# Optimization experiments

Measured on AMD Instinct MI355X. Metric: run time of the kernel, lower is better.

Reference implementation:

```python
import jax, jax.numpy as jnp
import numpy as np

IOU_THR = 0.5
SCORE_THR = 0.5
MAX_DET = 100
B, N, C = 16, 25200, 80


def setup_inputs() -> dict:
    key = jax.random.key(0)
    k1, k2, k3 = jax.random.split(key, 3)
    return {
        "boxes_xywh": jax.random.uniform(k1, (B, N, 4), dtype=jnp.float32),
        "objectness": jax.random.uniform(k2, (B, N, 1), dtype=jnp.float32),
        "class_prob": jax.random.uniform(k3, (B, N, C), dtype=jnp.float32),
    }


def _xywh_to_corners(b):
    x, y, w, h = jnp.split(b, 4, axis=-1)
    return jnp.concatenate([x - w / 2, y - h / 2, x + w / 2, y + h / 2], axis=-1)


def _broadcast_iou(box, boxes):
    # box [4], boxes [N,4] in x1,y1,x2,y2
    lt = jnp.maximum(box[:2], boxes[:, :2])
    rb = jnp.minimum(box[2:], boxes[:, 2:])
    wh = jnp.clip(rb - lt, 0.0)
    inter = wh[:, 0] * wh[:, 1]
    a1 = (box[2] - box[0]) * (box[3] - box[1])
    a2 = (boxes[:, 2] - boxes[:, 0]) * (boxes[:, 3] - boxes[:, 1])
    return inter / (a1 + a2 - inter + 1e-9)


def _nms_single(cand):
    # cand: [N, 4+1+C] rows = (x1,y1,x2,y2, score, class_probs...)
    n, d = cand.shape
    scores = cand[:, 4]
    active0 = scores >= SCORE_THR

    def body(i, state):
        active, out, count = state
        masked = jnp.where(active, scores, -jnp.inf)
        best = jnp.argmax(masked)
        valid = jnp.any(active)
        best_box = cand[best]
        out = out.at[i].set(jnp.where(valid, best_box, out[i]))
        count = count + valid.astype(jnp.int32)
        iou = _broadcast_iou(best_box[:4], cand[:, :4])
        keep = active & (iou <= IOU_THR)
        keep = keep.at[best].set(False)
        active = jnp.where(valid, keep, active)
        return active, out, count

    out0 = jnp.zeros((MAX_DET, d), cand.dtype)
    _, out, count = jax.lax.fori_loop(0, MAX_DET, body, (active0, out0, jnp.int32(0)))
    return out, count


def reference(boxes_xywh, objectness, class_prob):
    corners = _xywh_to_corners(boxes_xywh)  # [B,N,4]
    combined = jnp.concatenate([corners, objectness, class_prob], axis=-1)  # [B,N,5+C]
    final_result, count = jax.vmap(_nms_single)(combined)  # [B,MAX_DET,5+C], [B]
    nms_boxes = final_result[..., 0:4]
    nms_scores = final_result[..., 4:5]
    nms_classes = final_result[..., 5:]
    valid_count = count.astype(jnp.int32)[:, None]  # [B,1]
    return nms_boxes, nms_scores, nms_classes, valid_count
```

## Files before the change

kernel.cpp:

```cpp
#include <hip/hip_runtime.h>

#define NBOX    25200
#define NQ4     6300
#define NBATCH  16
#define NCLS    80
#define MAXDET  100
#define NBUCKET 1024
#define CAP     13824
#define SCORE_THR 0.5f
#define IOU_THR   0.5f
#define NGROUP  16
#define LAZY_BKT 896

__device__ __forceinline__ void mk_corners(float x, float y, float w, float h,
                                           float& x1, float& y1, float& x2, float& y2) {
#pragma clang fp contract(off)
    float hw = w * 0.5f;
    float hh = h * 0.5f;
    x1 = x - hw; y1 = y - hh; x2 = x + hw; y2 = y + hh;
}

__device__ __forceinline__ float areaf(float x1, float y1, float x2, float y2) {
#pragma clang fp contract(off)
    return (x2 - x1) * (y2 - y1);
}

__device__ __forceinline__ bool iou_gt(float kx1, float ky1, float kx2, float ky2, float ka,
                                       float cx1, float cy1, float cx2, float cy2, float ca) {
#pragma clang fp contract(off)
    float lx = fmaxf(kx1, cx1);
    float ly = fmaxf(ky1, cy1);
    float rx = fminf(kx2, cx2);
    float ry = fminf(ky2, cy2);
    float w  = fmaxf(rx - lx, 0.0f);
    float h  = fmaxf(ry - ly, 0.0f);
    float inter = w * h;
    float denom = ka + ca - inter + 1e-9f;
    return (inter / denom) > IOU_THR;
}

__device__ __forceinline__ float readlane_f(float v, int j) {
    return __uint_as_float((unsigned)__builtin_amdgcn_readlane((int)__float_as_uint(v), j));
}

__device__ __forceinline__ unsigned score_key(float s) {
    return __float_as_uint(s) - 0x3F000000u;
}

__global__ __launch_bounds__(1024)
void nms_kernel(const float* __restrict__ boxes_xywh,
                const float* __restrict__ objectness,
                const float* __restrict__ class_prob,
                float* __restrict__ out) {
    __shared__ unsigned s_hist[NBUCKET];
    __shared__ unsigned s_start[NBUCKET];
    __shared__ unsigned s_a[CAP];
    __shared__ unsigned s_b[CAP];
    __shared__ float4   s_kbox[MAXDET];
    __shared__ unsigned s_kept_idx[MAXDET];
    __shared__ unsigned s_wsum[16];
    __shared__ unsigned s_woff[16];
    __shared__ int      s_count;

    const int b = blockIdx.x;
    const int t = threadIdx.x;
    const int w = t >> 6;
    const int l = t & 63;
    const float* obj = objectness + (size_t)b * NBOX;
    const float* bx  = boxes_xywh + (size_t)b * NBOX * 4;

    float4 r[7];
#pragma unroll
    for (int i = 0; i < 7; ++i) {
        int n4 = t + (i << 10);
        if (n4 < NQ4) r[i] = *(const float4*)(obj + n4 * 4);
    }

    s_hist[t] = 0u;
    __syncthreads();
#pragma unroll
    for (int i = 0; i < 7; ++i) {
        int n4 = t + (i << 10);
        if (n4 < NQ4) {
            float sv[4] = {r[i].x, r[i].y, r[i].z, r[i].w};
#pragma unroll
            for (int u = 0; u < 4; ++u) {
                if (sv[u] >= SCORE_THR) {
                    unsigned bkt = score_key(sv[u]) >> 13;
                    if (bkt > 1023u) bkt = 1023u;
                    atomicAdd(&s_hist[bkt], 1u);
                }
            }
        }
    }
    __syncthreads();

    {
        unsigned f = s_hist[1023 - t];
        unsigned v = f;
#pragma unroll
        for (int off = 1; off < 64; off <<= 1) {
            unsigned u = (unsigned)__shfl_up((int)v, off);
            if (l >= off) v += u;
        }
        if (l == 63) s_wsum[w] = v;
        __syncthreads();
        if (t < 64) {
            unsigned x = (t < 16) ? s_wsum[t] : 0u;
            unsigned y = x;
#pragma unroll
            for (int off = 1; off < 16; off <<= 1) {
                unsigned u = (unsigned)__shfl_up((int)y, off);
                if (t >= off) y += u;
            }
            if (t < 16) s_woff[t] = y - x;
        }
        __syncthreads();
        s_start[1023 - t] = v - f + s_woff[w];
    }
    if (t == 0) s_count = 0;
    __syncthreads();

#pragma unroll
    for (int i = 0; i < 7; ++i) {
        int n4 = t + (i << 10);
        if (n4 < NQ4) {
            float sv[4] = {r[i].x, r[i].y, r[i].z, r[i].w};
#pragma unroll
            for (int u = 0; u < 4; ++u) {
                if (sv[u] >= SCORE_THR) {
                    unsigned ekey = score_key(sv[u]);
                    unsigned bkt  = ekey >> 13;
                    if (bkt > 1023u) bkt = 1023u;
                    if (bkt >= LAZY_BKT) {
                        int n = n4 * 4 + u;
                        unsigned el = ekey & 0x1FFFu;
                        unsigned pos = atomicAdd(&s_start[bkt], 1u);
                        if (pos < CAP)
                            s_a[pos] = (el << 18) | (0x3FFFFu - (unsigned)n);
                    }
                }
            }
        }
    }
    __syncthreads();

    auto sort_bucket = [&](int bkt) {
        unsigned h = s_hist[bkt];
        if (h == 0u) return;
        unsigned end = s_start[bkt];
        unsigned hi  = (end > CAP) ? CAP : end;
        unsigned lo  = (end >= h) ? end - h : 0u;
        if (lo > hi) lo = hi;
        unsigned sz = hi - lo;
        if (sz == 0u) return;
        if (sz <= 64u) {
            unsigned v = (l < (int)sz) ? s_a[lo + (unsigned)l] : 0u;
            int rank = 0;
            for (unsigned j = 0; j < sz; ++j)
                rank += ((unsigned)__shfl((int)v, (int)j) > v) ? 1 : 0;
            if (l < (int)sz) s_b[lo + (unsigned)rank] = v;
        } else {
            for (unsigned bb = 0; bb < sz; bb += 64u) {
                bool valid = bb + (unsigned)l < sz;
                unsigned v = valid ? s_a[lo + bb + (unsigned)l] : 0u;
                int rank = 0;
                for (unsigned j = 0; j < sz; ++j)
                    rank += (s_a[lo + j] > v) ? 1 : 0;
                if (valid) s_b[lo + (unsigned)rank] = v;
            }
        }
    };

    for (int bkt = (1023 - 63) + w; bkt <= 1023; bkt += 16) sort_bucket(bkt);
    __syncthreads();

    int count = 0;
    int nscat = 2;
    for (int g = 0; g < NGROUP; ++g) {
        const int BH = 1023 - (g << 6);
        const int BL = BH - 63;

        if (g >= nscat) {
            for (int n4 = t; n4 < NQ4; n4 += 1024) {
                float4 s4 = *(const float4*)(obj + n4 * 4);
                float sv[4] = {s4.x, s4.y, s4.z, s4.w};
#pragma unroll
                for (int u = 0; u < 4; ++u) {
                    if (sv[u] >= SCORE_THR) {
                        unsigned ekey = score_key(sv[u]);
                        unsigned bkt  = ekey >> 13;
                        if (bkt > 1023u) bkt = 1023u;
                        if (bkt < LAZY_BKT) {
                            int n = n4 * 4 + u;
                            unsigned el = ekey & 0x1FFFu;
                            unsigned pos = atomicAdd(&s_start[bkt], 1u);
                            if (pos < CAP)
                                s_a[pos] = (el << 18) | (0x3FFFFu - (unsigned)n);
                        }
                    }
                }
            }
            __syncthreads();
            nscat = NGROUP;
            for (int bkt = BL + w; bkt <= BH; bkt += 16) sort_bucket(bkt);
            __syncthreads();
        }

        if (w == 0) {
            unsigned glo = (g == 0) ? 0u : s_start[BH + 1];
            unsigned ghi = s_start[BL];
            if (glo > CAP) glo = CAP;
            if (ghi > CAP) ghi = CAP;

            if (glo < ghi && count < MAXDET) {
                unsigned aidx, bidx; float4 aq, bq; float asc, bsc;
                auto loadc = [&](unsigned cb, unsigned& ix, float4& q, float& sc) {
                    ix = 0u; q = make_float4(0.f, 0.f, 0.f, 0.f); sc = 0.f;
                    unsigned p0 = cb + (unsigned)l;
                    if (p0 < ghi) {
                        unsigned p = s_b[p0];
                        ix = 0x3FFFFu - (p & 0x3FFFFu);
                        q = *(const float4*)(bx + (size_t)ix * 4);
                        sc = obj[ix];
                    }
                };
                loadc(glo, aidx, aq, asc);
                loadc(glo + 64u, bidx, bq, bsc);

                for (unsigned base = glo; base < ghi && count < MAXDET; base += 64u) {
                    unsigned cidx = aidx; float4 cq = aq; float csc = asc;
                    aidx = bidx; aq = bq; asc = bsc;
                    loadc(base + 128u, bidx, bq, bsc);

                    int m = (int)(ghi - base); if (m > 64) m = 64;
                    float cx1, cy1, cx2, cy2;
                    mk_corners(cq.x, cq.y, cq.z, cq.w, cx1, cy1, cx2, cy2);
                    float ca = areaf(cx1, cy1, cx2, cy2);

                    bool sup = (l >= m);
                    int k = 0;
                    for (; k + 4 <= count; k += 4) {
                        float4 kb0 = s_kbox[k],     kb1 = s_kbox[k + 1];
                        float4 kb2 = s_kbox[k + 2], kb3 = s_kbox[k + 3];
                        sup = sup | iou_gt(kb0.x, kb0.y, kb0.z, kb0.w,
                                           areaf(kb0.x, kb0.y, kb0.z, kb0.w), cx1, cy1, cx2, cy2, ca);
                        sup = sup | iou_gt(kb1.x, kb1.y, kb1.z, kb1.w,
                                           areaf(kb1.x, kb1.y, kb1.z, kb1.w), cx1, cy1, cx2, cy2, ca);
                        sup = sup | iou_gt(kb2.x, kb2.y, kb2.z, kb2.w,
                                           areaf(kb2.x, kb2.y, kb2.z, kb2.w), cx1, cy1, cx2, cy2, ca);
                        sup = sup | iou_gt(kb3.x, kb3.y, kb3.z, kb3.w,
                                           areaf(kb3.x, kb3.y, kb3.z, kb3.w), cx1, cy1, cx2, cy2, ca);
                    }
                    for (; k < count; ++k) {
                        float4 kb = s_kbox[k];
                        sup = sup | iou_gt(kb.x, kb.y, kb.z, kb.w,
                                           areaf(kb.x, kb.y, kb.z, kb.w), cx1, cy1, cx2, cy2, ca);
                    }
                    unsigned long long act = __ballot(!sup);

                    unsigned long long accmask = 0ull;
                    const int cbase = count;
                    while (act != 0ull && count < MAXDET) {
                        int j = (int)__builtin_ctzll(act);
                        accmask |= 1ull << j;
                        float bx1 = readlane_f(cx1, j), by1 = readlane_f(cy1, j);
                        float bx2 = readlane_f(cx2, j), by2 = readlane_f(cy2, j);
                        float bar = readlane_f(ca, j);
                        bool su = iou_gt(bx1, by1, bx2, by2, bar, cx1, cy1, cx2, cy2, ca);
                        ++count;
                        act &= ~(1ull << j);
                        act &= ~__ballot(su);
                    }

                    if (accmask & (1ull << l)) {
                        int slot = cbase + (int)__popcll(accmask & ((1ull << l) - 1ull));
                        s_kbox[slot] = make_float4(cx1, cy1, cx2, cy2);
                        s_kept_idx[slot] = cidx;
                        float* ob = out + ((size_t)b * MAXDET + slot) * 4;
                        ob[0] = cx1; ob[1] = cy1; ob[2] = cx2; ob[3] = cy2;
                        out[NBATCH * MAXDET * 4 + b * MAXDET + slot] = csc;
                    }
                    __asm__ volatile("s_waitcnt lgkmcnt(0)" ::: "memory");
                }
            }
            if (l == 0) s_count = count;
        } else if (g + 1 < NGROUP && g + 1 < nscat) {
            const int BH2 = BH - 64, BL2 = BH2 - 63;
            for (int bkt = BL2 + (w - 1); bkt <= BH2; bkt += 15) sort_bucket(bkt);
        }
        __syncthreads();
        if (s_count >= MAXDET) break;
    }

    const int cf = s_count;
    for (int e = t; e < MAXDET * 4; e += 1024) {
        if ((e >> 2) >= cf) out[(size_t)b * MAXDET * 4 + e] = 0.0f;
    }
    for (int i = t; i < MAXDET; i += 1024) {
        if (i >= cf) out[NBATCH * MAXDET * 4 + b * MAXDET + i] = 0.0f;
    }
    const float* cp = class_prob + (size_t)b * NBOX * NCLS;
    float* oc = out + NBATCH * MAXDET * 5 + (size_t)b * MAXDET * NCLS;
    for (int e = t; e < cf * NCLS; e += 1024) {
        int i = e / NCLS;
        int c = e - i * NCLS;
        oc[e] = cp[(size_t)s_kept_idx[i] * NCLS + c];
    }
    for (int e = t + cf * NCLS; e < MAXDET * NCLS; e += 1024) oc[e] = 0.0f;
    if (t == 0)
        out[NBATCH * MAXDET * 5 + NBATCH * MAXDET * NCLS + b] = (float)cf;
}

extern "C" void kernel_launch(void* const* d_in, const int* in_sizes, int n_in,
                              void* d_out, int out_size, void* d_ws, size_t ws_size,
                              hipStream_t stream) {
    const float* boxes = (const float*)d_in[0];
    const float* objn  = (const float*)d_in[1];
    const float* clsp  = (const float*)d_in[2];
    float* out = (float*)d_out;
    nms_kernel<<<dim3(NBATCH), dim3(1024), 0, stream>>>(boxes, objn, clsp, out);
}
```

Baseline: 198.3 us.

## Stage sorted candidate boxes into shared memory during bucket sort

The bucket sort now writes back into s_a in place and, for each sorted candidate, gathers its box from global memory, converts it to corners and stores corners, score and index into double-buffered shared staging arrays. The serial NMS wave then reads candidates from LDS instead of doing dependent global loads in its critical path, and the score is rebuilt from the sort key rather than reloaded. Large buckets are ranked with register shuffles in chunks, capped at 320 elements, instead of repeated LDS scans. This moves global gather latency onto the parallel sorting waves but uses more LDS, and the 320 cap silently truncates oversized buckets.

```diff
diff --git a/kernel.cpp b/kernel.cpp
--- a/kernel.cpp
+++ b/kernel.cpp
@@ -11,6 +11,7 @@
 #define IOU_THR   0.5f
 #define NGROUP  16
 #define LAZY_BKT 896
+#define STAGECAP 1152
 
 __device__ __forceinline__ void mk_corners(float x, float y, float w, float h,
                                            float& x1, float& y1, float& x2, float& y2) {
@@ -55,7 +56,9 @@
     __shared__ unsigned s_hist[NBUCKET];
     __shared__ unsigned s_start[NBUCKET];
     __shared__ unsigned s_a[CAP];
-    __shared__ unsigned s_b[CAP];
+    __shared__ float4   s_cc[2][STAGECAP];
+    __shared__ float    s_cs[2][STAGECAP];
+    __shared__ unsigned s_ci[2][STAGECAP];
     __shared__ float4   s_kbox[MAXDET];
     __shared__ unsigned s_kept_idx[MAXDET];
     __shared__ unsigned s_wsum[16];
@@ -134,18 +137,17 @@
                     if (bkt > 1023u) bkt = 1023u;
                     if (bkt >= LAZY_BKT) {
                         int n = n4 * 4 + u;
-                        unsigned el = ekey & 0x1FFFu;
                         unsigned pos = atomicAdd(&s_start[bkt], 1u);
                         if (pos < CAP)
-                            s_a[pos] = (el << 18) | (0x3FFFFu - (unsigned)n);
-                    }
-                }
-            }
-        }
-    }
-    __syncthreads();
-
-    auto sort_bucket = [&](int bkt) {
+                            s_a[pos] = ((ekey & 0x1FFFu) << 18) | (0x3FFFFu - (unsigned)n);
+                    }
+                }
+            }
+        }
+    }
+    __syncthreads();
+
+    auto sort_stage = [&](int bkt, unsigned gbase, int buf) {
         unsigned h = s_hist[bkt];
         if (h == 0u) return;
         unsigned end = s_start[bkt];
@@ -159,20 +161,61 @@
             int rank = 0;
             for (unsigned j = 0; j < sz; ++j)
                 rank += ((unsigned)__shfl((int)v, (int)j) > v) ? 1 : 0;
-            if (l < (int)sz) s_b[lo + (unsigned)rank] = v;
+            if (l < (int)sz) {
+                s_a[lo + (unsigned)rank] = v;
+                unsigned spos = lo + (unsigned)rank - gbase;
+                if (spos < STAGECAP) {
+                    unsigned idx = 0x3FFFFu - (v & 0x3FFFFu);
+                    float4 q = *(const float4*)(bx + (size_t)idx * 4);
+                    float x1, y1, x2, y2;
+                    mk_corners(q.x, q.y, q.z, q.w, x1, y1, x2, y2);
+                    s_cc[buf][spos] = make_float4(x1, y1, x2, y2);
+                    s_cs[buf][spos] = __uint_as_float(0x3F000000u +
+                                        (((unsigned)bkt << 13) | (v >> 18)));
+                    s_ci[buf][spos] = idx;
+                }
+            }
         } else {
-            for (unsigned bb = 0; bb < sz; bb += 64u) {
-                bool valid = bb + (unsigned)l < sz;
-                unsigned v = valid ? s_a[lo + bb + (unsigned)l] : 0u;
-                int rank = 0;
-                for (unsigned j = 0; j < sz; ++j)
-                    rank += (s_a[lo + j] > v) ? 1 : 0;
-                if (valid) s_b[lo + (unsigned)rank] = v;
+            if (sz > 320u) sz = 320u;
+            unsigned v[5]; int rk[5];
+            int nch = (int)((sz + 63u) >> 6);
+#pragma unroll
+            for (int c = 0; c < 5; ++c) {
+                unsigned p = (unsigned)(c * 64 + l);
+                v[c] = (c < nch && p < sz) ? s_a[lo + p] : 0u;
+                rk[c] = 0;
+            }
+            for (int c2 = 0; c2 < nch; ++c2) {
+                for (int j = 0; j < 64; ++j) {
+                    unsigned o = (unsigned)__shfl((int)v[c2], j);
+                    bool val = (unsigned)(c2 * 64 + j) < sz;
+#pragma unroll
+                    for (int c = 0; c < 5; ++c)
+                        rk[c] += (val && o > v[c]) ? 1 : 0;
+                }
+            }
+#pragma unroll
+            for (int c = 0; c < 5; ++c) {
+                unsigned p = (unsigned)(c * 64 + l);
+                if (c < nch && p < sz) {
+                    s_a[lo + (unsigned)rk[c]] = v[c];
+                    unsigned spos = lo + (unsigned)rk[c] - gbase;
+                    if (spos < STAGECAP) {
+                        unsigned idx = 0x3FFFFu - (v[c] & 0x3FFFFu);
+                        float4 q = *(const float4*)(bx + (size_t)idx * 4);
+                        float x1, y1, x2, y2;
+                        mk_corners(q.x, q.y, q.z, q.w, x1, y1, x2, y2);
+                        s_cc[buf][spos] = make_float4(x1, y1, x2, y2);
+                        s_cs[buf][spos] = __uint_as_float(0x3F000000u +
+                                            (((unsigned)bkt << 13) | (v[c] >> 18)));
+                        s_ci[buf][spos] = idx;
+                    }
+                }
             }
         }
     };
 
-    for (int bkt = (1023 - 63) + w; bkt <= 1023; bkt += 16) sort_bucket(bkt);
+    for (int bkt = 960 + w; bkt <= 1023; bkt += 16) sort_stage(bkt, 0u, 0);
     __syncthreads();
 
     int count = 0;
@@ -193,17 +236,18 @@
                         if (bkt > 1023u) bkt = 1023u;
                         if (bkt < LAZY_BKT) {
                             int n = n4 * 4 + u;
-                            unsigned el = ekey & 0x1FFFu;
                             unsigned pos = atomicAdd(&s_start[bkt], 1u);
                             if (pos < CAP)
-                                s_a[pos] = (el << 18) | (0x3FFFFu - (unsigned)n);
+                                s_a[pos] = ((ekey & 0x1FFFu) << 18) | (0x3FFFFu - (unsigned)n);
                         }
                     }
                 }
             }
             __syncthreads();
             nscat = NGROUP;
-            for (int bkt = BL + w; bkt <= BH; bkt += 16) sort_bucket(bkt);
+            unsigned gb = s_start[BH + 1];
+            if (gb > CAP) gb = CAP;
+            for (int bkt = BL + w; bkt <= BH; bkt += 16) sort_stage(bkt, gb, g & 1);
             __syncthreads();
         }
 
@@ -212,82 +256,89 @@
             unsigned ghi = s_start[BL];
             if (glo > CAP) glo = CAP;
             if (ghi > CAP) ghi = CAP;
-
-            if (glo < ghi && count < MAXDET) {
-                unsigned aidx, bidx; float4 aq, bq; float asc, bsc;
-                auto loadc = [&](unsigned cb, unsigned& ix, float4& q, float& sc) {
-                    ix = 0u; q = make_float4(0.f, 0.f, 0.f, 0.f); sc = 0.f;
-                    unsigned p0 = cb + (unsigned)l;
-                    if (p0 < ghi) {
-                        unsigned p = s_b[p0];
-                        ix = 0x3FFFFu - (p & 0x3FFFFu);
-                        q = *(const float4*)(bx + (size_t)ix * 4);
-                        sc = obj[ix];
-                    }
-                };
-                loadc(glo, aidx, aq, asc);
-                loadc(glo + 64u, bidx, bq, bsc);
-
-                for (unsigned base = glo; base < ghi && count < MAXDET; base += 64u) {
-                    unsigned cidx = aidx; float4 cq = aq; float csc = asc;
-                    aidx = bidx; aq = bq; asc = bsc;
-                    loadc(base + 128u, bidx, bq, bsc);
-
-                    int m = (int)(ghi - base); if (m > 64) m = 64;
-                    float cx1, cy1, cx2, cy2;
-                    mk_corners(cq.x, cq.y, cq.z, cq.w, cx1, cy1, cx2, cy2);
-                    float ca = areaf(cx1, cy1, cx2, cy2);
-
-                    bool sup = (l >= m);
-                    int k = 0;
-                    for (; k + 4 <= count; k += 4) {
-                        float4 kb0 = s_kbox[k],     kb1 = s_kbox[k + 1];
-                        float4 kb2 = s_kbox[k + 2], kb3 = s_kbox[k + 3];
-                        sup = sup | iou_gt(kb0.x, kb0.y, kb0.z, kb0.w,
-                                           areaf(kb0.x, kb0.y, kb0.z, kb0.w), cx1, cy1, cx2, cy2, ca);
-                        sup = sup | iou_gt(kb1.x, kb1.y, kb1.z, kb1.w,
-                                           areaf(kb1.x, kb1.y, kb1.z, kb1.w), cx1, cy1, cx2, cy2, ca);
-                        sup = sup | iou_gt(kb2.x, kb2.y, kb2.z, kb2.w,
-                                           areaf(kb2.x, kb2.y, kb2.z, kb2.w), cx1, cy1, cx2, cy2, ca);
-                        sup = sup | iou_gt(kb3.x, kb3.y, kb3.z, kb3.w,
-                                           areaf(kb3.x, kb3.y, kb3.z, kb3.w), cx1, cy1, cx2, cy2, ca);
-                    }
-                    for (; k < count; ++k) {
-                        float4 kb = s_kbox[k];
-                        sup = sup | iou_gt(kb.x, kb.y, kb.z, kb.w,
-                                           areaf(kb.x, kb.y, kb.z, kb.w), cx1, cy1, cx2, cy2, ca);
-                    }
-                    unsigned long long act = __ballot(!sup);
-
-                    unsigned long long accmask = 0ull;
-                    const int cbase = count;
-                    while (act != 0ull && count < MAXDET) {
-                        int j = (int)__builtin_ctzll(act);
-                        accmask |= 1ull << j;
-                        float bx1 = readlane_f(cx1, j), by1 = readlane_f(cy1, j);
-                        float bx2 = readlane_f(cx2, j), by2 = readlane_f(cy2, j);
-                        float bar = readlane_f(ca, j);
-                        bool su = iou_gt(bx1, by1, bx2, by2, bar, cx1, cy1, cx2, cy2, ca);
-                        ++count;
-                        act &= ~(1ull << j);
-                        act &= ~__ballot(su);
-                    }
-
-                    if (accmask & (1ull << l)) {
-                        int slot = cbase + (int)__popcll(accmask & ((1ull << l) - 1ull));
-                        s_kbox[slot] = make_float4(cx1, cy1, cx2, cy2);
-                        s_kept_idx[slot] = cidx;
-                        float* ob = out + ((size_t)b * MAXDET + slot) * 4;
-                        ob[0] = cx1; ob[1] = cy1; ob[2] = cx2; ob[3] = cy2;
-                        out[NBATCH * MAXDET * 4 + b * MAXDET + slot] = csc;
-                    }
-                    __asm__ volatile("s_waitcnt lgkmcnt(0)" ::: "memory");
-                }
+            const int buf = g & 1;
+            const int gsz = (int)(ghi - glo);
+
+            for (int lb = 0; lb < gsz && count < MAXDET; lb += 64) {
+                int m = gsz - lb; if (m > 64) m = 64;
+                const int sp = lb + l;
+                const bool valid  = l < m;
+                const bool staged = sp < STAGECAP;
+                float cx1 = 0.f, cy1 = 0.f, cx2 = 0.f, cy2 = 0.f;
+                if (valid) {
+                    if (staged) {
+                        float4 cc = s_cc[buf][sp];
+                        cx1 = cc.x; cy1 = cc.y; cx2 = cc.z; cy2 = cc.w;
+                    } else {
+                        unsigned v = s_a[glo + (unsigned)sp];
+                        unsigned idx = 0x3FFFFu - (v & 0x3FFFFu);
+                        float4 q = *(const float4*)(bx + (size_t)idx * 4);
+                        mk_corners(q.x, q.y, q.z, q.w, cx1, cy1, cx2, cy2);
+                    }
+                }
+                float ca = areaf(cx1, cy1, cx2, cy2);
+
+                bool sup = !valid;
+                int k = 0;
+                for (; k + 4 <= count; k += 4) {
+                    float4 kb0 = s_kbox[k],     kb1 = s_kbox[k + 1];
+                    float4 kb2 = s_kbox[k + 2], kb3 = s_kbox[k + 3];
+                    sup = sup | iou_gt(kb0.x, kb0.y, kb0.z, kb0.w,
+                                       areaf(kb0.x, kb0.y, kb0.z, kb0.w), cx1, cy1, cx2, cy2, ca);
+                    sup = sup | iou_gt(kb1.x, kb1.y, kb1.z, kb1.w,
+                                       areaf(kb1.x, kb1.y, kb1.z, kb1.w), cx1, cy1, cx2, cy2, ca);
+                    sup = sup | iou_gt(kb2.x, kb2.y, kb2.z, kb2.w,
+                                       areaf(kb2.x, kb2.y, kb2.z, kb2.w), cx1, cy1, cx2, cy2, ca);
+                    sup = sup | iou_gt(kb3.x, kb3.y, kb3.z, kb3.w,
+                                       areaf(kb3.x, kb3.y, kb3.z, kb3.w), cx1, cy1, cx2, cy2, ca);
+                }
+                for (; k < count; ++k) {
+                    float4 kb = s_kbox[k];
+                    sup = sup | iou_gt(kb.x, kb.y, kb.z, kb.w,
+                                       areaf(kb.x, kb.y, kb.z, kb.w), cx1, cy1, cx2, cy2, ca);
+                }
+                unsigned long long act = __ballot(!sup);
+
+                unsigned long long accmask = 0ull;
+                const int cbase = count;
+                while (act != 0ull && count < MAXDET) {
+                    int j = (int)__builtin_ctzll(act);
+                    accmask |= 1ull << j;
+                    float bx1 = readlane_f(cx1, j), by1 = readlane_f(cy1, j);
+                    float bx2 = readlane_f(cx2, j), by2 = readlane_f(cy2, j);
+                    float bar = readlane_f(ca, j);
+                    bool su = iou_gt(bx1, by1, bx2, by2, bar, cx1, cy1, cx2, cy2, ca);
+                    ++count;
+                    act &= ~(1ull << j);
+                    act &= ~__ballot(su);
+                }
+
+                if (accmask & (1ull << l)) {
+                    int slot = cbase + (int)__popcll(accmask & ((1ull << l) - 1ull));
+                    unsigned cidx; float csc;
+                    if (staged) {
+                        cidx = s_ci[buf][sp];
+                        csc  = s_cs[buf][sp];
+                    } else {
+                        unsigned v = s_a[glo + (unsigned)sp];
+                        cidx = 0x3FFFFu - (v & 0x3FFFFu);
+                        csc  = obj[cidx];
+                    }
+                    s_kbox[slot] = make_float4(cx1, cy1, cx2, cy2);
+                    s_kept_idx[slot] = cidx;
+                    float* ob = out + ((size_t)b * MAXDET + slot) * 4;
+                    ob[0] = cx1; ob[1] = cy1; ob[2] = cx2; ob[3] = cy2;
+                    out[NBATCH * MAXDET * 4 + b * MAXDET + slot] = csc;
+                }
+                __asm__ volatile("s_waitcnt lgkmcnt(0)" ::: "memory");
             }
             if (l == 0) s_count = count;
         } else if (g + 1 < NGROUP && g + 1 < nscat) {
             const int BH2 = BH - 64, BL2 = BH2 - 63;
-            for (int bkt = BL2 + (w - 1); bkt <= BH2; bkt += 15) sort_bucket(bkt);
+            unsigned gb = s_start[BL];
+            if (gb > CAP) gb = CAP;
+            for (int bkt = BL2 + (w - 1); bkt <= BH2; bkt += 15)
+                sort_stage(bkt, gb, (g + 1) & 1);
         }
         __syncthreads();
         if (s_count >= MAXDET) break;
```

After: 203.3 us. 2.5% more time.
